# Performance work log

Measured on AMD Instinct MI355X. Metric: run time of the kernel, lower is better.

## Reference

```python
import jax, jax.numpy as jnp
from jax import lax
import numpy as np

B, T, I, H, FC = 1024, 512, 16, 50, 64


def _lstm_layer(x, w_ih, w_hh, b_ih, b_hh):
    """PyTorch-semantics single LSTM layer, batch_first. x: [B,T,in]. Returns h-seq [B,T,H]."""
    b = x.shape[0]
    h_dim = w_hh.shape[1]
    # Precompute input contribution for all timesteps in one big GEMM: [B,T,4H]
    gates_x = jnp.einsum('bti,gi->btg', x, w_ih) + b_ih + b_hh

    def step(carry, gx):
        h, c = carry
        g = gx + h @ w_hh.T                      # [B,4H]; gate order i,f,g,o (PyTorch)
        i_g, f_g, g_g, o_g = jnp.split(g, 4, axis=-1)
        i_g = jax.nn.sigmoid(i_g)
        f_g = jax.nn.sigmoid(f_g)
        g_g = jnp.tanh(g_g)
        o_g = jax.nn.sigmoid(o_g)
        c = f_g * c + i_g * g_g
        h = o_g * jnp.tanh(c)
        return (h, c), h

    h0 = jnp.zeros((b, h_dim), x.dtype)
    (_, _), hs = lax.scan(step, (h0, h0), jnp.swapaxes(gates_x, 0, 1))  # time-major scan
    return jnp.swapaxes(hs, 0, 1)


def setup_inputs() -> dict:
    key = jax.random.key(0)
    ks = jax.random.split(key, 14)
    s_i = 1.0 / np.sqrt(H)  # PyTorch LSTM init: U(-1/sqrt(H), 1/sqrt(H))
    u = lambda k, shape, s: jax.random.uniform(k, shape, jnp.float32, -s, s)
    return {
        'x': jax.random.normal(ks[0], (B, T, I), jnp.float32),
        'w_ih0': u(ks[1], (4 * H, I), s_i),
        'w_hh0': u(ks[2], (4 * H, H), s_i),
        'b_ih0': u(ks[3], (4 * H,), s_i),
        'b_hh0': u(ks[4], (4 * H,), s_i),
        'w_ih1': u(ks[5], (4 * H, H), s_i),
        'w_hh1': u(ks[6], (4 * H, H), s_i),
        'b_ih1': u(ks[7], (4 * H,), s_i),
        'b_hh1': u(ks[8], (4 * H,), s_i),
        'fc1_w': u(ks[9], (FC, H), 1.0 / np.sqrt(H)),
        'fc1_b': u(ks[10], (FC,), 1.0 / np.sqrt(H)),
        'fc2_w': u(ks[11], (1, FC), 1.0 / np.sqrt(FC)),
        'fc2_b': u(ks[12], (1,), 1.0 / np.sqrt(FC)),
    }


def reference(x, w_ih0, w_hh0, b_ih0, b_hh0, w_ih1, w_hh1, b_ih1, b_hh1,
              fc1_w, fc1_b, fc2_w, fc2_b):
    h1 = _lstm_layer(x, w_ih0, w_hh0, b_ih0, b_hh0)    # [B,T,H]
    h2 = _lstm_layer(h1, w_ih1, w_hh1, b_ih1, b_hh1)   # [B,T,H]
    last = h2[:, -1, :]                                 # [B,H]
    hidden = jax.nn.relu(last @ fc1_w.T + fc1_b)        # dropout is identity at inference
    return hidden @ fc2_w.T + fc2_b                     # [B,1]
```

## Files before the change

### kernel.cpp

```cpp
#include <hip/hip_runtime.h>

#define B_    1024
#define T_    512
#define I_    16
#define H_    50
#define FC_   64
#define HALFW 28
#define HP    56

typedef float v2f __attribute__((ext_vector_type(2)));

__device__ __forceinline__ float frcp(float x)   { return __builtin_amdgcn_rcpf(x); }
__device__ __forceinline__ float sigm(float x)   { return frcp(1.0f + __expf(-x)); }
__device__ __forceinline__ float tanh_f(float x) { return 1.0f - 2.0f * frcp(1.0f + __expf(2.0f * x)); }
__device__ __forceinline__ v2f   fma2(v2f a, v2f b, v2f c) { return __builtin_elementwise_fma(a, b, c); }
__device__ __forceinline__ v2f   mk2(float a, float b) { v2f r; r.x = a; r.y = b; return r; }

__device__ __forceinline__ float dpp_xor1(float v) {
    return __int_as_float(__builtin_amdgcn_update_dpp(0, __float_as_int(v), 0xB1, 0xF, 0xF, true));
}
__device__ __forceinline__ float dpp_xor2(float v) {
    return __int_as_float(__builtin_amdgcn_update_dpp(0, __float_as_int(v), 0x4E, 0xF, 0xF, true));
}

#define PKDOT(acc, W, kk, hv) { acc = fma2(W[2*(kk)],   mk2(hv.x, hv.y), acc); \
                                acc = fma2(W[2*(kk)+1], mk2(hv.z, hv.w), acc); }
#define XDOT(acc, Wj, v0, v1) { acc = fma2(Wj[0], mk2(v0.x, v0.y), acc); \
                                acc = fma2(Wj[1], mk2(v0.z, v0.w), acc); \
                                acc = fma2(Wj[2], mk2(v1.x, v1.y), acc); \
                                acc = fma2(Wj[3], mk2(v1.z, v1.w), acc); }

__global__ __launch_bounds__(256, 2) void lstm_pk(
    const float* __restrict__ x,
    const float* __restrict__ w_ih0, const float* __restrict__ w_hh0,
    const float* __restrict__ b_ih0, const float* __restrict__ b_hh0,
    const float* __restrict__ w_ih1, const float* __restrict__ w_hh1,
    const float* __restrict__ b_ih1, const float* __restrict__ b_hh1,
    const float* __restrict__ fc1_w, const float* __restrict__ fc1_b,
    const float* __restrict__ fc2_w, const float* __restrict__ fc2_b,
    float* __restrict__ out)
{
    __shared__ float h0s[2][2][HP];
    __shared__ float h1s[2][2][HP];

    const int tid  = threadIdx.x;
    const int u    = tid >> 2;
    const int qp   = (tid >> 1) & 1;
    const int s    = tid & 1;
    const bool gl  = tid < 4 * H_;
    const int row0 = blockIdx.x * 2;

    const float qa = qp ? 2.0f : -1.0f;
    const float qb = qp ? 1.0f :  0.0f;
    const float qm = qp ? -2.0f : 1.0f;

    v2f w0x[2][4], w0h[2][14], w1x[2][14], w1h[2][14];
    float bias0[2] = {0.f, 0.f}, bias1[2] = {0.f, 0.f};
    if (gl) {
        #pragma unroll
        for (int j = 0; j < 2; ++j) {
            const int g = (2 * qp + j) * H_ + u;
            #pragma unroll
            for (int k = 0; k < 4; ++k)
                w0x[j][k] = mk2(w_ih0[g * I_ + s * 8 + 2 * k],
                                w_ih0[g * I_ + s * 8 + 2 * k + 1]);
            #pragma unroll
            for (int k = 0; k < 14; ++k) {
                const int j0 = s * HALFW + 2 * k, j1 = j0 + 1;
                const bool v0 = j0 < H_, v1 = j1 < H_;
                w0h[j][k] = mk2(v0 ? w_hh0[g * H_ + j0] : 0.f, v1 ? w_hh0[g * H_ + j1] : 0.f);
                w1x[j][k] = mk2(v0 ? w_ih1[g * H_ + j0] : 0.f, v1 ? w_ih1[g * H_ + j1] : 0.f);
                w1h[j][k] = mk2(v0 ? w_hh1[g * H_ + j0] : 0.f, v1 ? w_hh1[g * H_ + j1] : 0.f);
            }
            if (s == 0) {
                bias0[j] = b_ih0[g] + b_hh0[g];
                bias1[j] = b_ih1[g] + b_hh1[g];
            }
        }
    }

    if (tid < 224) { ((float*)h0s)[tid] = 0.f; ((float*)h1s)[tid] = 0.f; }
    float c0[2] = {0.f, 0.f}, c1[2] = {0.f, 0.f};
    __syncthreads();

    auto cell = [&](v2f A0, v2f A1, float& c) -> float {
        float p0 = A0.x + A0.y;  p0 += dpp_xor1(p0);
        float p1 = A1.x + A1.y;  p1 += dpp_xor1(p1);
        float act0 = qb + qm * frcp(1.0f + __expf(qa * p0));
        float act1 = sigm(p1);
        float ox0 = dpp_xor2(act0);
        float ox1 = dpp_xor2(act1);
        float gi = qp ? ox0 : act0;
        float gf = qp ? ox1 : act1;
        float gg = qp ? act0 : ox0;
        float go = qp ? act1 : ox1;
        c = gf * c + gi * gg;
        return go * tanh_f(c);
    };

    if (gl) {
        #pragma unroll
        for (int r = 0; r < 2; ++r) {
            const float* xp = x + (size_t)(row0 + r) * T_ * I_ + s * 8;
            float4 xv0 = *(const float4*)xp;
            float4 xv1 = *(const float4*)(xp + 4);
            v2f a0 = mk2(bias0[0], 0.f), a1 = mk2(bias0[1], 0.f);
            XDOT(a0, w0x[0], xv0, xv1);
            XDOT(a1, w0x[1], xv0, xv1);
            float hv = cell(a0, a1, c0[r]);
            if ((tid & 3) == 0) h0s[0][r][u] = hv;
        }
    }
    __syncthreads();

    #pragma unroll 2
    for (int t = 0; t < T_ - 1; ++t) {
        const int pp = t & 1, pn = pp ^ 1;
        if (gl) {
            float4 xv[2][2];
            #pragma unroll
            for (int r = 0; r < 2; ++r) {
                const float* xp = x + ((size_t)(row0 + r) * T_ + (t + 1)) * I_ + s * 8;
                xv[r][0] = *(const float4*)xp;
                xv[r][1] = *(const float4*)(xp + 4);
            }
            #pragma unroll
            for (int r = 0; r < 2; ++r) {
                const float4* h0p = (const float4*)(&h0s[pp][r][s * HALFW]);
                const float4* h1p = (const float4*)(&h1s[pn][r][s * HALFW]);
                v2f A0 = mk2(bias1[0], 0.f), A1 = mk2(bias1[1], 0.f);
                v2f B0 = mk2(bias0[0], 0.f), B1 = mk2(bias0[1], 0.f);
                #pragma unroll
                for (int k = 0; k < 7; ++k) {
                    float4 hv = h0p[k];
                    PKDOT(A0, w1x[0], k, hv); PKDOT(A1, w1x[1], k, hv);
                    PKDOT(B0, w0h[0], k, hv); PKDOT(B1, w0h[1], k, hv);
                }
                #pragma unroll
                for (int k = 0; k < 7; ++k) {
                    float4 hv = h1p[k];
                    PKDOT(A0, w1h[0], k, hv); PKDOT(A1, w1h[1], k, hv);
                }
                XDOT(B0, w0x[0], xv[r][0], xv[r][1]);
                XDOT(B1, w0x[1], xv[r][0], xv[r][1]);
                float h1v = cell(A0, A1, c1[r]);
                float h0v = cell(B0, B1, c0[r]);
                if ((tid & 3) == 0) { h1s[pp][r][u] = h1v; h0s[pn][r][u] = h0v; }
            }
        }
        __syncthreads();
    }

    if (gl) {
        #pragma unroll
        for (int r = 0; r < 2; ++r) {
            const float4* h0p = (const float4*)(&h0s[1][r][s * HALFW]);
            const float4* h1p = (const float4*)(&h1s[0][r][s * HALFW]);
            v2f A0 = mk2(bias1[0], 0.f), A1 = mk2(bias1[1], 0.f);
            #pragma unroll
            for (int k = 0; k < 7; ++k) {
                float4 hv = h0p[k];
                PKDOT(A0, w1x[0], k, hv); PKDOT(A1, w1x[1], k, hv);
            }
            #pragma unroll
            for (int k = 0; k < 7; ++k) {
                float4 hv = h1p[k];
                PKDOT(A0, w1h[0], k, hv); PKDOT(A1, w1h[1], k, hv);
            }
            float h1v = cell(A0, A1, c1[r]);
            if ((tid & 3) == 0) h1s[1][r][u] = h1v;
        }
    }
    __syncthreads();

    if (tid < 2 * FC_) {
        const int r = tid >> 6, f = tid & 63;
        const float* hf = h1s[1][r];
        float a = fc1_b[f];
        #pragma unroll
        for (int j = 0; j < H_; ++j) a += fc1_w[f * H_ + j] * hf[j];
        float v = fmaxf(a, 0.f) * fc2_w[f];
        #pragma unroll
        for (int off = 1; off < FC_; off <<= 1) v += __shfl_xor(v, off);
        if (f == 0) out[row0 + r] = v + fc2_b[0];
    }
}

extern "C" void kernel_launch(void* const* d_in, const int* in_sizes, int n_in,
                              void* d_out, int out_size, void* d_ws, size_t ws_size,
                              hipStream_t stream) {
    const float* x     = (const float*)d_in[0];
    const float* w_ih0 = (const float*)d_in[1];
    const float* w_hh0 = (const float*)d_in[2];
    const float* b_ih0 = (const float*)d_in[3];
    const float* b_hh0 = (const float*)d_in[4];
    const float* w_ih1 = (const float*)d_in[5];
    const float* w_hh1 = (const float*)d_in[6];
    const float* b_ih1 = (const float*)d_in[7];
    const float* b_hh1 = (const float*)d_in[8];
    const float* fc1_w = (const float*)d_in[9];
    const float* fc1_b = (const float*)d_in[10];
    const float* fc2_w = (const float*)d_in[11];
    const float* fc2_b = (const float*)d_in[12];
    float* out = (float*)d_out;

    dim3 grid(B_ / 2), block(256);
    hipLaunchKernelGGL(lstm_pk, grid, block, 0, stream,
                       x, w_ih0, w_hh0, b_ih0, b_hh0,
                       w_ih1, w_hh1, b_ih1, b_hh1,
                       fc1_w, fc1_b, fc2_w, fc2_b, out);
}
```

Before: 974.7 us.

## Split each LSTM gate dot product four ways with one batch row per block

Each block now handles a single batch row with 448 threads, 8 threads per hidden unit. The per-unit dot products are split into four quarter-K slices and reduced with two DPP steps, and gate pairs are exchanged with a ds_swizzle xor-4. Before, each block processed two rows with 256 threads and half-K slices. The aim is to shorten the serial FMA chain per thread in the latency-bound recurrent step by doubling the threads that work on it. In exchange it adds an extra cross-lane reduction, more waves per block, and twice as many blocks.

```diff
diff --git a/kernel.cpp b/kernel.cpp
--- a/kernel.cpp
+++ b/kernel.cpp
@@ -5,7 +5,7 @@
 #define I_    16
 #define H_    50
 #define FC_   64
-#define HALFW 28
+#define QW    14
 #define HP    56
 
 typedef float v2f __attribute__((ext_vector_type(2)));
@@ -22,15 +22,11 @@
 __device__ __forceinline__ float dpp_xor2(float v) {
     return __int_as_float(__builtin_amdgcn_update_dpp(0, __float_as_int(v), 0x4E, 0xF, 0xF, true));
 }
+__device__ __forceinline__ float swz4(float v) {
+    return __int_as_float(__builtin_amdgcn_ds_swizzle(__float_as_int(v), 0x101F));
+}
 
-#define PKDOT(acc, W, kk, hv) { acc = fma2(W[2*(kk)],   mk2(hv.x, hv.y), acc); \
-                                acc = fma2(W[2*(kk)+1], mk2(hv.z, hv.w), acc); }
-#define XDOT(acc, Wj, v0, v1) { acc = fma2(Wj[0], mk2(v0.x, v0.y), acc); \
-                                acc = fma2(Wj[1], mk2(v0.z, v0.w), acc); \
-                                acc = fma2(Wj[2], mk2(v1.x, v1.y), acc); \
-                                acc = fma2(Wj[3], mk2(v1.z, v1.w), acc); }
-
-__global__ __launch_bounds__(256, 2) void lstm_pk(
+__global__ __launch_bounds__(448, 4) void lstm_q4(
     const float* __restrict__ x,
     const float* __restrict__ w_ih0, const float* __restrict__ w_hh0,
     const float* __restrict__ b_ih0, const float* __restrict__ b_hh0,
@@ -40,33 +36,32 @@
     const float* __restrict__ fc2_w, const float* __restrict__ fc2_b,
     float* __restrict__ out)
 {
-    __shared__ float h0s[2][2][HP];
-    __shared__ float h1s[2][2][HP];
+    __shared__ float h0s[2][HP], h1s[2][HP];
 
-    const int tid  = threadIdx.x;
-    const int u    = tid >> 2;
-    const int qp   = (tid >> 1) & 1;
-    const int s    = tid & 1;
-    const bool gl  = tid < 4 * H_;
-    const int row0 = blockIdx.x * 2;
+    const int tid = threadIdx.x;
+    const int u   = tid >> 3;
+    const int qp  = (tid >> 2) & 1;
+    const int s   = tid & 3;
+    const bool gl = tid < 8 * H_;
+    const int row = blockIdx.x;
 
     const float qa = qp ? 2.0f : -1.0f;
     const float qb = qp ? 1.0f :  0.0f;
     const float qm = qp ? -2.0f : 1.0f;
 
-    v2f w0x[2][4], w0h[2][14], w1x[2][14], w1h[2][14];
+    v2f w0x[2][2], w0h[2][7], w1x[2][7], w1h[2][7];
     float bias0[2] = {0.f, 0.f}, bias1[2] = {0.f, 0.f};
     if (gl) {
         #pragma unroll
         for (int j = 0; j < 2; ++j) {
             const int g = (2 * qp + j) * H_ + u;
             #pragma unroll
-            for (int k = 0; k < 4; ++k)
-                w0x[j][k] = mk2(w_ih0[g * I_ + s * 8 + 2 * k],
-                                w_ih0[g * I_ + s * 8 + 2 * k + 1]);
+            for (int k = 0; k < 2; ++k)
+                w0x[j][k] = mk2(w_ih0[g * I_ + s * 4 + 2 * k],
+                                w_ih0[g * I_ + s * 4 + 2 * k + 1]);
             #pragma unroll
-            for (int k = 0; k < 14; ++k) {
-                const int j0 = s * HALFW + 2 * k, j1 = j0 + 1;
+            for (int k = 0; k < 7; ++k) {
+                const int j0 = s * QW + 2 * k, j1 = j0 + 1;
                 const bool v0 = j0 < H_, v1 = j1 < H_;
                 w0h[j][k] = mk2(v0 ? w_hh0[g * H_ + j0] : 0.f, v1 ? w_hh0[g * H_ + j1] : 0.f);
                 w1x[j][k] = mk2(v0 ? w_ih1[g * H_ + j0] : 0.f, v1 ? w_ih1[g * H_ + j1] : 0.f);
@@ -79,37 +74,34 @@
         }
     }
 
-    if (tid < 224) { ((float*)h0s)[tid] = 0.f; ((float*)h1s)[tid] = 0.f; }
-    float c0[2] = {0.f, 0.f}, c1[2] = {0.f, 0.f};
+    if (tid < 112) { ((float*)h0s)[tid] = 0.f; ((float*)h1s)[tid] = 0.f; }
+    float c0 = 0.f, c1 = 0.f;
     __syncthreads();
 
     auto cell = [&](v2f A0, v2f A1, float& c) -> float {
-        float p0 = A0.x + A0.y;  p0 += dpp_xor1(p0);
-        float p1 = A1.x + A1.y;  p1 += dpp_xor1(p1);
+        float p0 = A0.x + A0.y;  p0 += dpp_xor1(p0);  p0 += dpp_xor2(p0);
+        float p1 = A1.x + A1.y;  p1 += dpp_xor1(p1);  p1 += dpp_xor2(p1);
         float act0 = qb + qm * frcp(1.0f + __expf(qa * p0));
         float act1 = sigm(p1);
-        float ox0 = dpp_xor2(act0);
-        float ox1 = dpp_xor2(act1);
-        float gi = qp ? ox0 : act0;
-        float gf = qp ? ox1 : act1;
-        float gg = qp ? act0 : ox0;
-        float go = qp ? act1 : ox1;
+        float r0 = swz4(act0);
+        float r1 = swz4(act1);
+        float gi = qp ? r0 : act0;
+        float gf = qp ? r1 : act1;
+        float gg = qp ? act0 : r0;
+        float go = qp ? act1 : r1;
         c = gf * c + gi * gg;
         return go * tanh_f(c);
     };
 
     if (gl) {
-        #pragma unroll
-        for (int r = 0; r < 2; ++r) {
-            const float* xp = x + (size_t)(row0 + r) * T_ * I_ + s * 8;
-            float4 xv0 = *(const float4*)xp;
-            float4 xv1 = *(const float4*)(xp + 4);
-            v2f a0 = mk2(bias0[0], 0.f), a1 = mk2(bias0[1], 0.f);
-            XDOT(a0, w0x[0], xv0, xv1);
-            XDOT(a1, w0x[1], xv0, xv1);
-            float hv = cell(a0, a1, c0[r]);
-            if ((tid & 3) == 0) h0s[0][r][u] = hv;
-        }
+        const float4 xv = *(const float4*)(x + (size_t)row * T_ * I_ + s * 4);
+        v2f B0 = mk2(bias0[0], 0.f), B1 = mk2(bias0[1], 0.f);
+        B0 = fma2(w0x[0][0], mk2(xv.x, xv.y), B0);
+        B0 = fma2(w0x[0][1], mk2(xv.z, xv.w), B0);
+        B1 = fma2(w0x[1][0], mk2(xv.x, xv.y), B1);
+        B1 = fma2(w0x[1][1], mk2(xv.z, xv.w), B1);
+        float hv = cell(B0, B1, c0);
+        if ((tid & 7) == 0) h0s[0][u] = hv;
     }
     __syncthreads();
 
@@ -117,72 +109,61 @@
     for (int t = 0; t < T_ - 1; ++t) {
         const int pp = t & 1, pn = pp ^ 1;
         if (gl) {
-            float4 xv[2][2];
+            const float4 xv = *(const float4*)(x + ((size_t)row * T_ + (t + 1)) * I_ + s * 4);
+            const v2f* h0p = (const v2f*)&h0s[pp][s * QW];
+            const v2f* h1p = (const v2f*)&h1s[pn][s * QW];
+            v2f A0 = mk2(bias1[0], 0.f), A1 = mk2(bias1[1], 0.f);
+            v2f B0 = mk2(bias0[0], 0.f), B1 = mk2(bias0[1], 0.f);
             #pragma unroll
-            for (int r = 0; r < 2; ++r) {
-                const float* xp = x + ((size_t)(row0 + r) * T_ + (t + 1)) * I_ + s * 8;
-                xv[r][0] = *(const float4*)xp;
-                xv[r][1] = *(const float4*)(xp + 4);
+            for (int k = 0; k < 7; ++k) {
+                v2f hv = h0p[k];
+                A0 = fma2(w1x[0][k], hv, A0);  A1 = fma2(w1x[1][k], hv, A1);
+                B0 = fma2(w0h[0][k], hv, B0);  B1 = fma2(w0h[1][k], hv, B1);
             }
             #pragma unroll
-            for (int r = 0; r < 2; ++r) {
-                const float4* h0p = (const float4*)(&h0s[pp][r][s * HALFW]);
-                const float4* h1p = (const float4*)(&h1s[pn][r][s * HALFW]);
-                v2f A0 = mk2(bias1[0], 0.f), A1 = mk2(bias1[1], 0.f);
-                v2f B0 = mk2(bias0[0], 0.f), B1 = mk2(bias0[1], 0.f);
-                #pragma unroll
-                for (int k = 0; k < 7; ++k) {
-                    float4 hv = h0p[k];
-                    PKDOT(A0, w1x[0], k, hv); PKDOT(A1, w1x[1], k, hv);
-                    PKDOT(B0, w0h[0], k, hv); PKDOT(B1, w0h[1], k, hv);
-                }
-                #pragma unroll
-                for (int k = 0; k < 7; ++k) {
-                    float4 hv = h1p[k];
-                    PKDOT(A0, w1h[0], k, hv); PKDOT(A1, w1h[1], k, hv);
-                }
-                XDOT(B0, w0x[0], xv[r][0], xv[r][1]);
-                XDOT(B1, w0x[1], xv[r][0], xv[r][1]);
-                float h1v = cell(A0, A1, c1[r]);
-                float h0v = cell(B0, B1, c0[r]);
-                if ((tid & 3) == 0) { h1s[pp][r][u] = h1v; h0s[pn][r][u] = h0v; }
+            for (int k = 0; k < 7; ++k) {
+                v2f hv = h1p[k];
+                A0 = fma2(w1h[0][k], hv, A0);  A1 = fma2(w1h[1][k], hv, A1);
             }
+            B0 = fma2(w0x[0][0], mk2(xv.x, xv.y), B0);
+            B0 = fma2(w0x[0][1], mk2(xv.z, xv.w), B0);
+            B1 = fma2(w0x[1][0], mk2(xv.x, xv.y), B1);
+            B1 = fma2(w0x[1][1], mk2(xv.z, xv.w), B1);
+            float h1v = cell(A0, A1, c1);
+            float h0v = cell(B0, B1, c0);
+            if ((tid & 7) == 0) { h1s[pp][u] = h1v; h0s[pn][u] = h0v; }
         }
         __syncthreads();
     }
 
     if (gl) {
+        const v2f* h0p = (const v2f*)&h0s[1][s * QW];
+        const v2f* h1p = (const v2f*)&h1s[0][s * QW];
+        v2f A0 = mk2(bias1[0], 0.f), A1 = mk2(bias1[1], 0.f);
         #pragma unroll
-        for (int r = 0; r < 2; ++r) {
-            const float4* h0p = (const float4*)(&h0s[1][r][s * HALFW]);
-            const float4* h1p = (const float4*)(&h1s[0][r][s * HALFW]);
-            v2f A0 = mk2(bias1[0], 0.f), A1 = mk2(bias1[1], 0.f);
-            #pragma unroll
-            for (int k = 0; k < 7; ++k) {
-                float4 hv = h0p[k];
-                PKDOT(A0, w1x[0], k, hv); PKDOT(A1, w1x[1], k, hv);
-            }
-            #pragma unroll
-            for (int k = 0; k < 7; ++k) {
-                float4 hv = h1p[k];
-                PKDOT(A0, w1h[0], k, hv); PKDOT(A1, w1h[1], k, hv);
-            }
-            float h1v = cell(A0, A1, c1[r]);
-            if ((tid & 3) == 0) h1s[1][r][u] = h1v;
+        for (int k = 0; k < 7; ++k) {
+            v2f hv = h0p[k];
+            A0 = fma2(w1x[0][k], hv, A0);  A1 = fma2(w1x[1][k], hv, A1);
         }
+        #pragma unroll
+        for (int k = 0; k < 7; ++k) {
+            v2f hv = h1p[k];
+            A0 = fma2(w1h[0][k], hv, A0);  A1 = fma2(w1h[1][k], hv, A1);
+        }
+        float h1v = cell(A0, A1, c1);
+        if ((tid & 7) == 0) h1s[1][u] = h1v;
     }
     __syncthreads();
 
-    if (tid < 2 * FC_) {
-        const int r = tid >> 6, f = tid & 63;
-        const float* hf = h1s[1][r];
-        float a = fc1_b[f];
+    if (tid < FC_) {
+        const float* hf = h1s[1];
+        float a = fc1_b[tid];
         #pragma unroll
-        for (int j = 0; j < H_; ++j) a += fc1_w[f * H_ + j] * hf[j];
-        float v = fmaxf(a, 0.f) * fc2_w[f];
+        for (int j = 0; j < H_; ++j) a += fc1_w[tid * H_ + j] * hf[j];
+        float v = fmaxf(a, 0.f) * fc2_w[tid];
         #pragma unroll
         for (int off = 1; off < FC_; off <<= 1) v += __shfl_xor(v, off);
-        if (f == 0) out[row0 + r] = v + fc2_b[0];
+        if (tid == 0) out[row] = v + fc2_b[0];
     }
 }
 
@@ -204,8 +185,8 @@
     const float* fc2_b = (const float*)d_in[12];
     float* out = (float*)d_out;
 
-    dim3 grid(B_ / 2), block(256);
-    hipLaunchKernelGGL(lstm_pk, grid, block, 0, stream,
+    dim3 grid(B_), block(448);
+    hipLaunchKernelGGL(lstm_q4, grid, block, 0, stream,
                        x, w_ih0, w_hh0, b_ih0, b_hh0,
                        w_ih1, w_hh1, b_ih1, b_hh1,
                        fc1_w, fc1_b, fc2_w, fc2_b, out);
```

New measurement: 1.506 ms. +54.6%, slower.
